# Kernel optimization log

Measured on AMD Instinct MI355X. Metric: run time of the kernel, lower is better.

The kernel has to match this reference:

```python
import jax, jax.numpy as jnp
import numpy as np

EPS = 1e-6      # eps used in token2map / map2token weight normalization
LN_EPS = 1e-5   # torch nn.LayerNorm default


def layernorm(x, w, b):
    m = jnp.mean(x, axis=-1, keepdims=True)
    xc = x - m
    v = jnp.mean(xc * xc, axis=-1, keepdims=True)
    return xc * jax.lax.rsqrt(v + LN_EPS) * w + b


def grid_index(H_init, W_init, H, W):
    # nearest-neighbor map: flattened feature-map index for each init-grid cell
    r = (jnp.arange(H_init) * H) // H_init
    c = (jnp.arange(W_init) * W) // W_init
    return (r[:, None] * W + c[None, :]).reshape(-1)  # [N_init]


def token2map(x, idx_token, H, W, H_init, W_init):
    # tokens [B,N,C] -> feature map [B,H,W,C] via weighted scatter-mean
    B, N, C = x.shape
    idx_hw = grid_index(H_init, W_init, H, W)                    # [N_init]
    counts = jnp.zeros((H * W,), x.dtype).at[idx_hw].add(1.0)    # identical across batch
    w = (1.0 / (counts + EPS))[idx_hw]                           # [N_init]
    src = jnp.take_along_axis(x, idx_token[..., None], axis=1)   # [B,N_init,C]
    out = jnp.zeros((B, H * W, C), x.dtype).at[:, idx_hw, :].add(src * w[None, :, None])
    return out.reshape(B, H, W, C)


def map2token(fmap, idx_token, N, H_init, W_init):
    # feature map [B,H,W,C] -> tokens [B,N,C]: mean of member grid cells per token
    B, H, W, C = fmap.shape
    idx_hw = grid_index(H_init, W_init, H, W)
    bidx = jnp.arange(B)[:, None]
    counts = jnp.zeros((B, N), fmap.dtype).at[bidx, idx_token].add(1.0)
    wt = jnp.take_along_axis(1.0 / (counts + EPS), idx_token, axis=1)  # [B,N_init]
    src = fmap.reshape(B, H * W, C)[:, idx_hw, :]                      # [B,N_init,C]
    return jnp.zeros((B, N, C), fmap.dtype).at[bidx, idx_token].add(src * wt[..., None])


def _forward(x, token_score, idx_token,
             norm1_w, norm1_b, q_w, q_b, kv_w, kv_b, sr_w, sr_b, srn_w, srn_b,
             proj_w, proj_b, norm2_w, norm2_b, fc1_w, fc1_b, skip_w, dw_w, dw_b,
             fc2_w, fc2_b, H, W, H_init, W_init, token_num, num_heads):
    B, N, C = x.shape
    d = C // num_heads
    scale = d ** -0.5
    sr = 2  # sr_ratio

    xn = layernorm(x, norm1_w, norm1_b)  # q_dict['x'] = norm1(x); kv_dict is q_dict

    # ---- TCFormerDynamicAttention ----
    q = (xn @ q_w + q_b).reshape(B, N, num_heads, d).transpose(0, 2, 1, 3)  # [B,h,N,d]
    tmp = jnp.concatenate([xn, token_score], axis=-1)            # [B,N,C+1]
    tmp_map = token2map(tmp, idx_token, H, W, H_init, W_init)    # [B,H,W,C+1]
    kv_map, conf_map = tmp_map[..., :C], tmp_map[..., C]
    kv = jax.lax.conv_general_dilated(kv_map, sr_w, (sr, sr), 'VALID',
        dimension_numbers=('NHWC', 'HWIO', 'NHWC')) + sr_b       # sr conv, stride 2
    M = (H // sr) * (W // sr)
    kv = layernorm(kv.reshape(B, M, C), srn_w, srn_b)
    conf = conf_map.reshape(B, H // sr, sr, W // sr, sr).mean(axis=(2, 4)).reshape(B, M)

    kv = (kv @ kv_w + kv_b).reshape(B, M, 2, num_heads, d)
    k = kv[:, :, 0].transpose(0, 2, 1, 3)                        # [B,h,M,d]
    v = kv[:, :, 1].transpose(0, 2, 1, 3)
    attn = jnp.einsum('bhnd,bhmd->bhnm', q * scale, k) + conf[:, None, None, :]
    attn = jax.nn.softmax(attn, axis=-1)
    a = jnp.einsum('bhnm,bhmd->bhnd', attn, v).transpose(0, 2, 1, 3).reshape(B, N, C)
    x = x + (a @ proj_w + proj_b)

    # ---- TCMLP ----
    h = layernorm(x, norm2_w, norm2_b) @ fc1_w + fc1_b           # [B,N,H1]
    hmap = token2map(h, idx_token, H, W, H_init, W_init)         # [B,H,W,H1]
    hmap = jax.lax.conv_general_dilated(hmap, dw_w, (1, 1), ((1, 1), (1, 1)),
        dimension_numbers=('NHWC', 'HWIO', 'NHWC'),
        feature_group_count=h.shape[-1]) + dw_b                  # depthwise 3x3
    hc = h * skip_w + map2token(hmap, idx_token, N, H_init, W_init)  # skip = dw 1x1 conv1d
    hc = jax.nn.gelu(hc, approximate=False)
    return x + (hc @ fc2_w + fc2_b)


def setup_inputs() -> dict:
    B, N, C, H1 = 8, 1568, 256, 1024
    H = W = 56
    H_init = W_init = 112
    key = jax.random.key(0)
    ks = jax.random.split(key, 16)
    r = lambda i, shape, s=0.02: jax.random.normal(ks[i], shape, jnp.float32) * s
    return {
        'x': jax.random.normal(ks[0], (B, N, C), jnp.float32),
        'token_score': jax.random.normal(ks[1], (B, N, 1), jnp.float32),
        'idx_token': jax.random.randint(ks[2], (B, H_init * W_init), 0, N),
        'norm1_w': jnp.ones((C,), jnp.float32), 'norm1_b': jnp.zeros((C,), jnp.float32),
        'q_w': r(3, (C, C)), 'q_b': jnp.zeros((C,), jnp.float32),
        'kv_w': r(4, (C, 2 * C)), 'kv_b': jnp.zeros((2 * C,), jnp.float32),
        'sr_w': r(5, (2, 2, C, C)), 'sr_b': jnp.zeros((C,), jnp.float32),
        'srn_w': jnp.ones((C,), jnp.float32), 'srn_b': jnp.zeros((C,), jnp.float32),
        'proj_w': r(6, (C, C)), 'proj_b': jnp.zeros((C,), jnp.float32),
        'norm2_w': jnp.ones((C,), jnp.float32), 'norm2_b': jnp.zeros((C,), jnp.float32),
        'fc1_w': r(7, (C, H1)), 'fc1_b': jnp.zeros((H1,), jnp.float32),
        'skip_w': 1.0 + r(8, (H1,), 0.1),
        'dw_w': r(9, (3, 3, 1, H1), 0.1), 'dw_b': jnp.zeros((H1,), jnp.float32),
        'fc2_w': r(10, (H1, C)), 'fc2_b': jnp.zeros((C,), jnp.float32),
        'H': H, 'W': W, 'H_init': H_init, 'W_init': W_init,
        'token_num': N, 'num_heads': 8,
    }


def reference(x, token_score, idx_token, norm1_w, norm1_b, q_w, q_b, kv_w, kv_b,
              sr_w, sr_b, srn_w, srn_b, proj_w, proj_b, norm2_w, norm2_b,
              fc1_w, fc1_b, skip_w, dw_w, dw_b, fc2_w, fc2_b,
              H, W, H_init, W_init, token_num, num_heads):
    return _forward(x, token_score, idx_token, norm1_w, norm1_b, q_w, q_b, kv_w, kv_b,
                    sr_w, sr_b, srn_w, srn_b, proj_w, proj_b, norm2_w, norm2_b,
                    fc1_w, fc1_b, skip_w, dw_w, dw_b, fc2_w, fc2_b,
                    H, W, H_init, W_init, token_num, num_heads)
```

## Files before the change

kernel.cpp:

```cpp
#include <hip/hip_runtime.h>
#include <math.h>

#define BB 8
#define NTOK 1568
#define CD 256
#define HIMG 56
#define WIMG 56
#define HWSZ 3136
#define HIG 112
#define WIG 112
#define NI 12544
#define MKV 784
#define MPAD 800
#define NHEADS 8
#define HEADD 32
#define HH1 1024
#define ROWS1 (BB*NTOK)
#define ROWSK (BB*MKV)
#define LOG2E 1.4426950408889634f

typedef unsigned short bfu;
typedef __attribute__((ext_vector_type(4))) unsigned short bf4;
typedef __attribute__((ext_vector_type(8))) unsigned short bf8;
typedef __attribute__((ext_vector_type(8))) short s8v;
typedef __attribute__((ext_vector_type(4))) float f4v;
typedef __attribute__((ext_vector_type(16))) float f16v;

__device__ inline float b2f(bfu u) { union { unsigned i; float f; } x; x.i = (unsigned)u << 16; return x.f; }
__device__ inline bfu f2b(float f) {
  union { float f; unsigned i; } x; x.f = f;
  unsigned r = x.i + 0x7fffu + ((x.i >> 16) & 1u);
  return (bfu)(r >> 16);
}
__device__ inline int get_isb(const unsigned* probe) { return probe[0] == 0x3F803F80u ? 1 : 0; }
__device__ inline float ldd(const void* p, size_t i, int isb) {
  return isb ? b2f(((const bfu*)p)[i]) : ((const float*)p)[i];
}
__device__ inline int xswz(int wg, int nwg) {
  return (nwg & 7) ? wg : (wg & 7) * (nwg >> 3) + (wg >> 3);
}

__global__ __launch_bounds__(256) void wtr_tile(const void* __restrict__ w0,
                                                const void* __restrict__ w1,
                                                const void* __restrict__ w2,
                                                const void* __restrict__ w3,
                                                const void* __restrict__ w4,
                                                const void* __restrict__ w5,
                                                const void* __restrict__ w6,
                                                const void* __restrict__ w7,
                                                bfu* __restrict__ wtb,
                                                bfu* __restrict__ vt,
                                                float* __restrict__ conf,
                                                const unsigned* __restrict__ probe) {
  int isb = get_isb(probe);
  int bid = blockIdx.x, tid = threadIdx.x;
  if (bid >= 1064) {
    int t = (bid - 1064) * 256 + tid;
    int b = t / 4096, rem = t % 4096;
    int d = rem / 16, m = MKV + (rem % 16);
    vt[((size_t)(b * 256 + d)) * MPAD + m] = 0;
    if (t < 128) conf[(t / 16) * MPAD + MKV + (t % 16)] = -1e30f;
    return;
  }
  if (bid >= 1024) {
    int idx = (bid - 1024) * 256 + tid;
    if (idx < 9216) wtb[1048576 + idx] = f2b(ldd(w6, idx, isb));
    else            wtb[1048576 + idx] = f2b(ldd(w7, idx - 9216, isb));
    return;
  }
  const void* W; int K, N; bfu* Wt; int tloc;
  if (bid < 64)       { W = w0; K = 256;  N = 256;  Wt = wtb;          tloc = bid; }
  else if (bid < 320) { W = w1; K = 1024; N = 256;  Wt = wtb + 65536;  tloc = bid - 64; }
  else if (bid < 448) { W = w2; K = 256;  N = 512;  Wt = wtb + 327680; tloc = bid - 320; }
  else if (bid < 512) { W = w3; K = 256;  N = 256;  Wt = wtb + 458752; tloc = bid - 448; }
  else if (bid < 768) { W = w4; K = 256;  N = 1024; Wt = wtb + 524288; tloc = bid - 512; }
  else                { W = w5; K = 1024; N = 256;  Wt = wtb + 786432; tloc = bid - 768; }
  int ntn = N >> 5;
  int tn = tloc % ntn, tk = tloc / ntn;
  int n0 = tn * 32, k0 = tk * 32;
  __shared__ float s[32][33];
  int tx = tid & 31, ty = tid >> 5;
#pragma unroll
  for (int i = 0; i < 4; i++) {
    int k = ty + 8 * i;
    s[k][tx] = ldd(W, (size_t)(k0 + k) * N + n0 + tx, isb);
  }
  __syncthreads();
#pragma unroll
  for (int i = 0; i < 4; i++) {
    int n = ty + 8 * i;
    Wt[(size_t)(n0 + n) * K + k0 + tx] = f2b(s[tx][n]);
  }
}

__global__ __launch_bounds__(256) void ln_kernel(const void* __restrict__ in, int inmode,
                                                 const void* __restrict__ w,
                                                 const void* __restrict__ bta,
                                                 bfu* __restrict__ out,
                                                 const unsigned* __restrict__ probe) {
  int isb = get_isb(probe);
  int im = (inmode == 2) ? isb : inmode;
  int blk = xswz(blockIdx.x, gridDim.x);
  int wv = threadIdx.x >> 6, lane = threadIdx.x & 63;
  int row = blk * 4 + wv;
  int c4 = lane * 4;
  float v[4];
  if (im) {
    bf4 t = *(const bf4*)((const bfu*)in + (size_t)row * CD + c4);
#pragma unroll
    for (int j = 0; j < 4; j++) v[j] = b2f(t[j]);
  } else {
    float4 t = *(const float4*)((const float*)in + (size_t)row * CD + c4);
    v[0] = t.x; v[1] = t.y; v[2] = t.z; v[3] = t.w;
  }
  float s1 = v[0] + v[1] + v[2] + v[3];
  float s2 = v[0] * v[0] + v[1] * v[1] + v[2] * v[2] + v[3] * v[3];
#pragma unroll
  for (int off = 1; off < 64; off <<= 1) {
    s1 += __shfl_xor(s1, off);
    s2 += __shfl_xor(s2, off);
  }
  float m = s1 * (1.0f / CD);
  float inv = rsqrtf(s2 * (1.0f / CD) - m * m + 1e-5f);
  bf4 ov;
#pragma unroll
  for (int j = 0; j < 4; j++)
    ov[j] = f2b((v[j] - m) * inv * ldd(w, c4 + j, isb) + ldd(bta, c4 + j, isb));
  *(bf4*)(out + (size_t)row * CD + c4) = ov;
}

__global__ __launch_bounds__(256) void gemm2ph(const bfu* __restrict__ A,
                                               const bfu* __restrict__ Bt,
                                               const void* __restrict__ bias,
                                               const void* __restrict__ resid, int rmode,
                                               void* __restrict__ Cc, int cmode,
                                               void* __restrict__ aux,
                                               int K, int Ncols,
                                               const unsigned* __restrict__ probe) {
  int isb = get_isb(probe);
  int rm = (rmode == 1) ? (isb ? 3 : 2) : rmode;
  int cm = (cmode == 2) ? (isb ? 0 : 1) : cmode;
  __shared__ bfu As[2][64][40];
  __shared__ bfu Bs[2][64][40];
  int t = threadIdx.x;
  int nbx = Ncols >> 6;
  int id = xswz(blockIdx.x, gridDim.x);
  int row0 = (id / nbx) * 64, col0 = (id % nbx) * 64;
  int sr = t >> 2, sc = (t & 3) * 8;
  int w = t >> 6, lane = t & 63;
  int li = lane & 15, q = lane >> 4;
  int wm = w * 16;
  const bfu* pa = A + (size_t)(row0 + sr) * K + sc;
  const bfu* pb = Bt + (size_t)(col0 + sr) * K + sc;
  f4v zz = {0.f, 0.f, 0.f, 0.f};
  f4v acc[4];
#pragma unroll
  for (int ni = 0; ni < 4; ni++) acc[ni] = zz;
  s8v la = *(const s8v*)(pa);
  s8v lb = *(const s8v*)(pb);
  int cur = 0;
  for (int k0 = 32; k0 <= K; k0 += 32) {
    *(s8v*)(&As[cur][sr][sc]) = la;
    *(s8v*)(&Bs[cur][sr][sc]) = lb;
    __syncthreads();
    if (k0 < K) {
      la = *(const s8v*)(pa + k0);
      lb = *(const s8v*)(pb + k0);
    }
    s8v af  = *(const s8v*)(&As[cur][wm + li][q * 8]);
    s8v bf0 = *(const s8v*)(&Bs[cur][li][q * 8]);
    s8v bf1 = *(const s8v*)(&Bs[cur][16 + li][q * 8]);
    s8v bf2 = *(const s8v*)(&Bs[cur][32 + li][q * 8]);
    s8v bf3 = *(const s8v*)(&Bs[cur][48 + li][q * 8]);
    __builtin_amdgcn_s_setprio(1);
    acc[0] = __builtin_amdgcn_mfma_f32_16x16x32_bf16(af, bf0, acc[0], 0, 0, 0);
    acc[1] = __builtin_amdgcn_mfma_f32_16x16x32_bf16(af, bf1, acc[1], 0, 0, 0);
    acc[2] = __builtin_amdgcn_mfma_f32_16x16x32_bf16(af, bf2, acc[2], 0, 0, 0);
    acc[3] = __builtin_amdgcn_mfma_f32_16x16x32_bf16(af, bf3, acc[3], 0, 0, 0);
    __builtin_amdgcn_s_setprio(0);
    cur ^= 1;
  }
  float bw[4];
#pragma unroll
  for (int ni = 0; ni < 4; ni++) bw[ni] = ldd(bias, col0 + ni * 16 + li, isb);
#pragma unroll
  for (int ni = 0; ni < 4; ni++) {
    int col = col0 + ni * 16 + li;
#pragma unroll
    for (int r = 0; r < 4; r++) {
      int row = row0 + wm + q * 4 + r;
      size_t base = (size_t)row * Ncols + col;
      float v = acc[ni][r] + bw[ni];
      if (rm == 2) v += ((const float*)resid)[base];
      else if (rm == 3) v += b2f(((const bfu*)resid)[base]);
      if (cm == 0) ((bfu*)Cc)[base] = f2b(v);
      else if (cm == 1) ((float*)Cc)[base] = v;
      else {
        if (col < 256) ((bfu*)Cc)[base] = f2b(v);
        else {
          int bb = row / MKV, mm = row - bb * MKV;
          ((bfu*)aux)[((size_t)(bb * 256) + (col - 256)) * MPAD + mm] = f2b(v);
        }
      }
    }
  }
}

__global__ __launch_bounds__(256) void akv_kernel(const bfu* __restrict__ xn,
                                                  const void* __restrict__ tscore,
                                                  const int* __restrict__ idx_token,
                                                  bfu* __restrict__ Akv,
                                                  float* __restrict__ conf,
                                                  const unsigned* __restrict__ probe) {
  int isb = get_isb(probe);
  int blk = xswz(blockIdx.x, gridDim.x), tid = threadIdx.x;
  int b = blk / MKV, m = blk % MKV;
  int i2 = m / 28, j2 = m % 28;
  __shared__ int nn[16];
  __shared__ float cacc[16];
  if (tid < 16) {
    int a = (tid >> 3) & 1, kb = (tid >> 2) & 1, di = (tid >> 1) & 1, dj = tid & 1;
    int ti = 4 * i2 + 2 * a + di, tj = 4 * j2 + 2 * kb + dj;
    int n = idx_token[b * NI + ti * WIG + tj];
    nn[tid] = n;
    cacc[tid] = ldd(tscore, b * NTOK + n, isb);
  }
  __syncthreads();
  const float w4 = 1.0f / (4.0f + 1e-6f);
  int g = tid >> 6, c4 = (tid & 63) * 4;
  bf4 a0 = *(const bf4*)(xn + (size_t)(b * NTOK + nn[g * 4 + 0]) * CD + c4);
  bf4 a1 = *(const bf4*)(xn + (size_t)(b * NTOK + nn[g * 4 + 1]) * CD + c4);
  bf4 a2 = *(const bf4*)(xn + (size_t)(b * NTOK + nn[g * 4 + 2]) * CD + c4);
  bf4 a3 = *(const bf4*)(xn + (size_t)(b * NTOK + nn[g * 4 + 3]) * CD + c4);
  bf4 rv;
#pragma unroll
  for (int j = 0; j < 4; j++)
    rv[j] = f2b(w4 * (b2f(a0[j]) + b2f(a1[j]) + b2f(a2[j]) + b2f(a3[j])));
  *(bf4*)(Akv + (size_t)blk * 1024 + g * CD + c4) = rv;
  if (tid == 0) {
    float s = 0.f;
    for (int k = 0; k < 16; k++) s += cacc[k];
    conf[b * MPAD + m] = 0.25f * w4 * s * 5.656854249492381f;
  }
}

__global__ __launch_bounds__(256) void attn_kernel(const bfu* __restrict__ qb,
                                                   const bfu* __restrict__ kv,
                                                   const bfu* __restrict__ vt,
                                                   const float* __restrict__ conf,
                                                   bfu* __restrict__ out) {
  __shared__ float sdata[4][64][17];
  int tid = threadIdx.x;
  int w = tid >> 6, lane = tid & 63;
  int l31 = lane & 31, hi = lane >> 5;
  int blk = xswz(blockIdx.x, gridDim.x);
  int qt = blk % 25, tt = blk / 25;
  int hh = tt & 7, b = tt >> 3;
  int n0 = qt * 64;
  int two = (qt < 24);
  const bfu* qrow1 = qb + (size_t)(b * NTOK + n0 + l31) * CD + hh * HEADD + hi * 8;
  s8v qfA1 = *(const s8v*)(qrow1);
  s8v qfB1 = *(const s8v*)(qrow1 + 16);
  s8v qfA2 = {0, 0, 0, 0, 0, 0, 0, 0}, qfB2 = qfA2;
  if (two) {
    const bfu* qrow2 = qrow1 + (size_t)32 * CD;
    qfA2 = *(const s8v*)(qrow2);
    qfB2 = *(const s8v*)(qrow2 + 16);
  }
  const float scale = 0.17677669529663689f * LOG2E;
  const bfu* kbase = kv + hh * HEADD + hi * 8;
  const bfu* vbase = vt + ((size_t)(b * 256 + hh * HEADD + l31)) * MPAD + hi * 8;
  const float* cbase = conf + b * MPAD + 4 * hi;
  f16v oc1, oc2;
#pragma unroll
  for (int r = 0; r < 16; r++) { oc1[r] = 0.f; oc2[r] = 0.f; }
  float lr1 = 0.f, lr2 = 0.f;
  int w32 = w * 32;
  const bfu* kp0 = kbase + (size_t)(b * MKV + w32 + l31) * 512;
  s8v kfA = *(const s8v*)(kp0);
  s8v kfB = *(const s8v*)(kp0 + 16);
  s8v vfA = *(const s8v*)(vbase + w32);
  s8v vfB = *(const s8v*)(vbase + w32 + 16);
  float4 cf0 = *(const float4*)(cbase + w32);
  float4 cf1 = *(const float4*)(cbase + w32 + 8);
  float4 cf2 = *(const float4*)(cbase + w32 + 16);
  float4 cf3 = *(const float4*)(cbase + w32 + 24);
  for (int m0 = w32; m0 < MPAD; m0 += 128) {
    s8v ckA = kfA, ckB = kfB, cvA = vfA, cvB = vfB;
    float4 d0 = cf0, d1 = cf1, d2 = cf2, d3 = cf3;
    int m1 = m0 + 128;
    if (m1 < MPAD) {
      int mA = m1 + l31; if (mA > MKV - 1) mA = MKV - 1;
      const bfu* kp = kbase + (size_t)(b * MKV + mA) * 512;
      kfA = *(const s8v*)(kp);
      kfB = *(const s8v*)(kp + 16);
      vfA = *(const s8v*)(vbase + m1);
      vfB = *(const s8v*)(vbase + m1 + 16);
      cf0 = *(const float4*)(cbase + m1);
      cf1 = *(const float4*)(cbase + m1 + 8);
      cf2 = *(const float4*)(cbase + m1 + 16);
      cf3 = *(const float4*)(cbase + m1 + 24);
    }
    f16v cseed;
    cseed[0] = d0.x; cseed[1] = d0.y; cseed[2] = d0.z; cseed[3] = d0.w;
    cseed[4] = d1.x; cseed[5] = d1.y; cseed[6] = d1.z; cseed[7] = d1.w;
    cseed[8] = d2.x; cseed[9] = d2.y; cseed[10] = d2.z; cseed[11] = d2.w;
    cseed[12] = d3.x; cseed[13] = d3.y; cseed[14] = d3.z; cseed[15] = d3.w;
    __builtin_amdgcn_s_setprio(1);
    f16v c = __builtin_amdgcn_mfma_f32_32x32x16_bf16(ckA, qfA1, cseed, 0, 0, 0);
    c = __builtin_amdgcn_mfma_f32_32x32x16_bf16(ckB, qfB1, c, 0, 0, 0);
    __builtin_amdgcn_s_setprio(0);
    {
      float p[16], ps0 = 0.f, ps1 = 0.f, ps2 = 0.f, ps3 = 0.f;
#pragma unroll
      for (int r = 0; r < 16; r++) {
        p[r] = __builtin_amdgcn_exp2f(c[r] * scale);
        if ((r & 3) == 0) ps0 += p[r];
        else if ((r & 3) == 1) ps1 += p[r];
        else if ((r & 3) == 2) ps2 += p[r];
        else ps3 += p[r];
      }
      lr1 += (ps0 + ps1) + (ps2 + ps3);
      unsigned Z[8];
#pragma unroll
      for (int a2 = 0; a2 < 8; a2++)
        asm("v_cvt_pk_bf16_f32 %0, %1, %2" : "=v"(Z[a2]) : "v"(p[2 * a2]), "v"(p[2 * a2 + 1]));
      asm("v_permlane32_swap_b32 %0, %1" : "+v"(Z[0]), "+v"(Z[2]));
      asm("v_permlane32_swap_b32 %0, %1" : "+v"(Z[1]), "+v"(Z[3]));
      asm("v_permlane32_swap_b32 %0, %1" : "+v"(Z[4]), "+v"(Z[6]));
      asm("v_permlane32_swap_b32 %0, %1" : "+v"(Z[5]), "+v"(Z[7]));
      union { unsigned u[4]; s8v v; } B1, B2;
      B1.u[0] = Z[0]; B1.u[1] = Z[1]; B1.u[2] = Z[2]; B1.u[3] = Z[3];
      B2.u[0] = Z[4]; B2.u[1] = Z[5]; B2.u[2] = Z[6]; B2.u[3] = Z[7];
      __builtin_amdgcn_s_setprio(1);
      oc1 = __builtin_amdgcn_mfma_f32_32x32x16_bf16(cvA, B1.v, oc1, 0, 0, 0);
      oc1 = __builtin_amdgcn_mfma_f32_32x32x16_bf16(cvB, B2.v, oc1, 0, 0, 0);
      __builtin_amdgcn_s_setprio(0);
    }
    if (two) {
      __builtin_amdgcn_s_setprio(1);
      f16v c2 = __builtin_amdgcn_mfma_f32_32x32x16_bf16(ckA, qfA2, cseed, 0, 0, 0);
      c2 = __builtin_amdgcn_mfma_f32_32x32x16_bf16(ckB, qfB2, c2, 0, 0, 0);
      __builtin_amdgcn_s_setprio(0);
      float p[16], ps0 = 0.f, ps1 = 0.f, ps2 = 0.f, ps3 = 0.f;
#pragma unroll
      for (int r = 0; r < 16; r++) {
        p[r] = __builtin_amdgcn_exp2f(c2[r] * scale);
        if ((r & 3) == 0) ps0 += p[r];
        else if ((r & 3) == 1) ps1 += p[r];
        else if ((r & 3) == 2) ps2 += p[r];
        else ps3 += p[r];
      }
      lr2 += (ps0 + ps1) + (ps2 + ps3);
      unsigned Z[8];
#pragma unroll
      for (int a2 = 0; a2 < 8; a2++)
        asm("v_cvt_pk_bf16_f32 %0, %1, %2" : "=v"(Z[a2]) : "v"(p[2 * a2]), "v"(p[2 * a2 + 1]));
      asm("v_permlane32_swap_b32 %0, %1" : "+v"(Z[0]), "+v"(Z[2]));
      asm("v_permlane32_swap_b32 %0, %1" : "+v"(Z[1]), "+v"(Z[3]));
      asm("v_permlane32_swap_b32 %0, %1" : "+v"(Z[4]), "+v"(Z[6]));
      asm("v_permlane32_swap_b32 %0, %1" : "+v"(Z[5]), "+v"(Z[7]));
      union { unsigned u[4]; s8v v; } B1, B2;
      B1.u[0] = Z[0]; B1.u[1] = Z[1]; B1.u[2] = Z[2]; B1.u[3] = Z[3];
      B2.u[0] = Z[4]; B2.u[1] = Z[5]; B2.u[2] = Z[6]; B2.u[3] = Z[7];
      __builtin_amdgcn_s_setprio(1);
      oc2 = __builtin_amdgcn_mfma_f32_32x32x16_bf16(cvA, B1.v, oc2, 0, 0, 0);
      oc2 = __builtin_amdgcn_mfma_f32_32x32x16_bf16(cvB, B2.v, oc2, 0, 0, 0);
      __builtin_amdgcn_s_setprio(0);
    }
  }
#pragma unroll
  for (int r = 0; r < 16; r++) sdata[w][lane][r] = oc1[r];
  sdata[w][lane][16] = lr1;
  __syncthreads();
  if (w == 0) {
    float s[17];
#pragma unroll
    for (int r = 0; r < 17; r++)
      s[r] = sdata[0][lane][r] + sdata[1][lane][r] + sdata[2][lane][r] + sdata[3][lane][r];
    float l = s[16];
    l += __shfl_xor(l, 32);
    float inv = 1.0f / l;
    bfu* op = out + (size_t)(b * NTOK + n0 + l31) * CD + hh * HEADD + 4 * hi;
#pragma unroll
    for (int g = 0; g < 4; g++) {
      bf4 o;
#pragma unroll
      for (int u = 0; u < 4; u++) o[u] = f2b(s[4 * g + u] * inv);
      *(bf4*)(op + 8 * g) = o;
    }
  }
  if (two) {
    __syncthreads();
#pragma unroll
    for (int r = 0; r < 16; r++) sdata[w][lane][r] = oc2[r];
    sdata[w][lane][16] = lr2;
    __syncthreads();
    if (w == 0) {
      float s[17];
#pragma unroll
      for (int r = 0; r < 17; r++)
        s[r] = sdata[0][lane][r] + sdata[1][lane][r] + sdata[2][lane][r] + sdata[3][lane][r];
      float l = s[16];
      l += __shfl_xor(l, 32);
      float inv = 1.0f / l;
      bfu* op = out + (size_t)(b * NTOK + n0 + 32 + l31) * CD + hh * HEADD + 4 * hi;
#pragma unroll
      for (int g = 0; g < 4; g++) {
        bf4 o;
#pragma unroll
        for (int u = 0; u < 4; u++) o[u] = f2b(s[4 * g + u] * inv);
        *(bf4*)(op + 8 * g) = o;
      }
    }
  }
}

__global__ __launch_bounds__(128) void hmap_kernel(const bfu* __restrict__ h,
                                                   const int* __restrict__ idx_token,
                                                   bfu* __restrict__ hmap) {
  int blk = xswz(blockIdx.x, gridDim.x), tid = threadIdx.x;
  int b = blk / HWSZ, cell = blk % HWSZ;
  int i = cell / WIMG, j = cell % WIMG;
  __shared__ int nn[4];
  if (tid < 4) {
    int di = tid >> 1, dj = tid & 1;
    nn[tid] = idx_token[b * NI + (2 * i + di) * WIG + (2 * j + dj)];
  }
  __syncthreads();
  const float w4 = 1.0f / (4.0f + 1e-6f);
  int c8 = tid * 8;
  bf8 a0 = *(const bf8*)(h + (size_t)(b * NTOK + nn[0]) * HH1 + c8);
  bf8 a1 = *(const bf8*)(h + (size_t)(b * NTOK + nn[1]) * HH1 + c8);
  bf8 a2 = *(const bf8*)(h + (size_t)(b * NTOK + nn[2]) * HH1 + c8);
  bf8 a3 = *(const bf8*)(h + (size_t)(b * NTOK + nn[3]) * HH1 + c8);
  bf8 rv;
#pragma unroll
  for (int j2 = 0; j2 < 8; j2++)
    rv[j2] = f2b(w4 * (b2f(a0[j2]) + b2f(a1[j2]) + b2f(a2[j2]) + b2f(a3[j2])));
  *(bf8*)(hmap + (size_t)blk * HH1 + c8) = rv;
}

__global__ __launch_bounds__(256) void dw_kernel(const bfu* __restrict__ hmap,
                                                 const bfu* __restrict__ dwt,
                                                 const bfu* __restrict__ dbt,
                                                 bfu* __restrict__ dwout) {
  int blk = xswz(blockIdx.x, gridDim.x);
  int j4 = blk % 14; int rem = blk / 14;
  int i = rem % HIMG; int b = rem / HIMG;
  int tid = threadIdx.x;
  int c4 = tid * 4;
  int j0 = j4 * 4;
  float wf[9][4];
#pragma unroll
  for (int k = 0; k < 9; k++) {
    bf4 wv = *(const bf4*)(dwt + k * HH1 + c4);
#pragma unroll
    for (int u = 0; u < 4; u++) wf[k][u] = b2f(wv[u]);
  }
  bf4 bias = *(const bf4*)(dbt + c4);
  float bi[4];
#pragma unroll
  for (int u = 0; u < 4; u++) bi[u] = b2f(bias[u]);
  bf4 tp[3][6];
  const size_t bbase = (size_t)b * HWSZ;
#pragma unroll
  for (int r = 0; r < 3; r++) {
    int yy = i - 1 + r;
    bool rowok = (unsigned)yy < (unsigned)HIMG;
#pragma unroll
    for (int cc = 0; cc < 6; cc++) {
      int xx = j0 - 1 + cc;
      bf4 v = {0, 0, 0, 0};
      if (rowok && (unsigned)xx < (unsigned)WIMG)
        v = *(const bf4*)(hmap + (bbase + yy * WIMG + xx) * HH1 + c4);
      tp[r][cc] = v;
    }
  }
#pragma unroll
  for (int j = 0; j < 4; j++) {
    float acc[4] = {bi[0], bi[1], bi[2], bi[3]};
#pragma unroll
    for (int r = 0; r < 3; r++)
#pragma unroll
      for (int kx = 0; kx < 3; kx++) {
        bf4 hv = tp[r][j + kx];
#pragma unroll
        for (int u = 0; u < 4; u++) acc[u] += b2f(hv[u]) * wf[r * 3 + kx][u];
      }
    bf4 ov;
#pragma unroll
    for (int u = 0; u < 4; u++) ov[u] = f2b(acc[u]);
    *(bf4*)(dwout + (bbase + i * WIMG + j0 + j) * HH1 + c4) = ov;
  }
}

__global__ void count_kernel(const int* __restrict__ idx, int* __restrict__ cnt) {
  int t = xswz(blockIdx.x, gridDim.x) * 256 + threadIdx.x;
  int b = t / NI;
  atomicAdd(&cnt[b * NTOK + idx[t]], 1);
}
__global__ __launch_bounds__(256) void scan_kernel(const int* __restrict__ cnt, int2* __restrict__ co) {
  int b = blockIdx.x, tid = threadIdx.x;
  __shared__ int s[NTOK];
  for (int i = tid; i < NTOK; i += 256) s[i] = cnt[b * NTOK + i];
  __syncthreads();
  for (int st = 1; st < NTOK; st <<= 1) {
    int vals[7]; int k = 0;
    for (int i = tid; i < NTOK; i += 256, k++) vals[k] = (i >= st) ? s[i - st] : 0;
    __syncthreads();
    k = 0;
    for (int i = tid; i < NTOK; i += 256, k++) s[i] += vals[k];
    __syncthreads();
  }
  for (int i = tid; i < NTOK; i += 256) {
    int2 v; v.x = cnt[b * NTOK + i]; v.y = (i > 0) ? s[i - 1] : 0;
    co[b * NTOK + i] = v;
  }
}
__global__ void fill_kernel(const int* __restrict__ idx, const int2* __restrict__ co,
                            int* __restrict__ cursor, int* __restrict__ tlist) {
  int t = xswz(blockIdx.x, gridDim.x) * 256 + threadIdx.x;
  int b = t / NI, tt = t % NI;
  int n = idx[t];
  int p = atomicAdd(&cursor[b * NTOK + n], 1);
  tlist[b * NI + co[b * NTOK + n].y + p] = tt;
}

__global__ __launch_bounds__(128) void m2t_kernel(const bfu* __restrict__ h,
                                                  const bfu* __restrict__ dwout,
                                                  const int2* __restrict__ co,
                                                  const int* __restrict__ tlist,
                                                  const void* __restrict__ skipw,
                                                  bfu* __restrict__ hc,
                                                  const unsigned* __restrict__ probe) {
  int isb = get_isb(probe);
  int blk = xswz(blockIdx.x, gridDim.x), tid = threadIdx.x;
  int lane = tid & 63;
  int b = blk / NTOK, n = blk % NTOK;
  int c8 = tid * 8;
  bf8 hv = *(const bf8*)(h + (size_t)blk * HH1 + c8);
  int2 cv = co[b * NTOK + n];
  int c = cv.x, o0 = cv.y;
  float inv = 1.0f / ((float)c + 1e-6f);
  float a[8] = {};
  for (int k0 = 0; k0 < c; k0 += 16) {
    int kk = k0 + (lane & 15);
    int e = 0;
    if (kk < c) e = tlist[b * NI + o0 + kk];
    bf8 dv[16];
#pragma unroll
    for (int j = 0; j < 16; j++) {
      if (k0 + j < c) {
        int tt = __shfl(e, j);
        int ti = tt / WIG, tj = tt % WIG;
        int cell = (ti >> 1) * WIMG + (tj >> 1);
        dv[j] = *(const bf8*)(dwout + ((size_t)b * HWSZ + cell) * HH1 + c8);
      }
    }
#pragma unroll
    for (int j = 0; j < 16; j++) {
      if (k0 + j < c) {
#pragma unroll
        for (int j2 = 0; j2 < 8; j2++) a[j2] += b2f(dv[j][j2]);
      }
    }
  }
  bf8 ov;
  const float is2 = 0.70710678118654752f;
#pragma unroll
  for (int j2 = 0; j2 < 8; j2++) {
    float r = b2f(hv[j2]) * ldd(skipw, c8 + j2, isb) + a[j2] * inv;
    r = 0.5f * r * (1.0f + erff(r * is2));
    ov[j2] = f2b(r);
  }
  *(bf8*)(hc + (size_t)blk * HH1 + c8) = ov;
}

extern "C" void kernel_launch(void* const* d_in, const int* in_sizes, int n_in,
                              void* d_out, int out_size, void* d_ws, size_t ws_size,
                              hipStream_t stream) {
  const void* x        = d_in[0];
  const void* tscore   = d_in[1];
  const int*  idx_tok  = (const int*)d_in[2];
  const void* norm1_w  = d_in[3];
  const void* norm1_b  = d_in[4];
  const void* q_w      = d_in[5];
  const void* q_b      = d_in[6];
  const void* kv_w     = d_in[7];
  const void* kv_b     = d_in[8];
  const void* sr_w     = d_in[9];
  const void* sr_b     = d_in[10];
  const void* srn_w    = d_in[11];
  const void* srn_b    = d_in[12];
  const void* proj_w   = d_in[13];
  const void* proj_b   = d_in[14];
  const void* norm2_w  = d_in[15];
  const void* norm2_b  = d_in[16];
  const void* fc1_w    = d_in[17];
  const void* fc1_b    = d_in[18];
  const void* skip_w   = d_in[19];
  const void* dw_w     = d_in[20];
  const void* dw_b     = d_in[21];
  const void* fc2_w    = d_in[22];
  const void* fc2_b    = d_in[23];
  const unsigned* probe = (const unsigned*)d_in[3];

  float* ws = (float*)d_ws;
  size_t o = 0;
  float* x2 = ws + o;          o += (size_t)ROWS1 * CD;
  float* hR = ws + o;          o += (size_t)ROWS1 * HH1 / 2;
  float* mR = ws + o;          o += (size_t)BB * HWSZ * HH1 / 2;
  float* dR = ws + o;          o += (size_t)BB * HWSZ * HH1 / 2;
  int* ibase = (int*)(ws + o); o += (size_t)(4 * ROWS1 + BB * NI);
  bfu* wtb   = (bfu*)(ws + o); o += 529408;
  bfu* vtb   = (bfu*)(ws + o);

  bfu* Akv   = (bfu*)hR;
  bfu* kvc   = (bfu*)(hR + (size_t)ROWSK * 1024 / 2);
  bfu* h     = (bfu*)hR;
  bfu* qbuf  = (bfu*)mR;
  bfu* kvout = (bfu*)(mR + (size_t)ROWS1 * CD / 2);
  float* conf  = mR + (size_t)ROWS1 * CD / 2 + (size_t)ROWSK * 512 / 2;
  bfu* hmap  = (bfu*)mR;
  bfu* hc    = (bfu*)mR;
  bfu* xn    = (bfu*)dR;
  bfu* dwout = (bfu*)dR;
  int* counts = ibase;
  int* cursor = ibase + ROWS1;
  int2* co2   = (int2*)(ibase + 2 * ROWS1);
  int* tlist  = ibase + 4 * ROWS1;
  bfu* q_wt    = wtb;
  bfu* sr_wt   = wtb + 65536;
  bfu* kv_wt   = wtb + 327680;
  bfu* proj_wt = wtb + 458752;
  bfu* fc1_wt  = wtb + 524288;
  bfu* fc2_wt  = wtb + 786432;
  bfu* dwt     = wtb + 1048576;
  bfu* dbt     = wtb + 1057792;

  wtr_tile<<<1192, 256, 0, stream>>>(q_w, sr_w, kv_w, proj_w, fc1_w, fc2_w, dw_w, dw_b,
                                     wtb, vtb, conf, probe);
  hipMemsetAsync(counts, 0, (size_t)(2 * ROWS1) * sizeof(int), stream);

  ln_kernel<<<ROWS1 / 4, 256, 0, stream>>>(x, 2, norm1_w, norm1_b, xn, probe);
  gemm2ph<<<784, 256, 0, stream>>>(xn, q_wt, q_b, nullptr, 0, qbuf, 0, nullptr, 256, 256, probe);
  akv_kernel<<<ROWSK, 256, 0, stream>>>(xn, tscore, idx_tok, Akv, conf, probe);
  gemm2ph<<<392, 256, 0, stream>>>(Akv, sr_wt, sr_b, nullptr, 0, kvc, 0, nullptr, 1024, 256, probe);
  ln_kernel<<<ROWSK / 4, 256, 0, stream>>>(kvc, 1, srn_w, srn_b, kvc, probe);
  gemm2ph<<<784, 256, 0, stream>>>(kvc, kv_wt, kv_b, nullptr, 0, kvout, 3, vtb, 256, 512, probe);
  attn_kernel<<<BB * NHEADS * 25, 256, 0, stream>>>(qbuf, kvout, vtb, conf, xn);
  gemm2ph<<<784, 256, 0, stream>>>(xn, proj_wt, proj_b, x, 1, x2, 1, nullptr, 256, 256, probe);
  ln_kernel<<<ROWS1 / 4, 256, 0, stream>>>(x2, 0, norm2_w, norm2_b, xn, probe);
  gemm2ph<<<3136, 256, 0, stream>>>(xn, fc1_wt, fc1_b, nullptr, 0, h, 0, nullptr, 256, 1024, probe);
  hmap_kernel<<<BB * HWSZ, 128, 0, stream>>>(h, idx_tok, hmap);
  dw_kernel<<<BB * HIMG * 14, 256, 0, stream>>>(hmap, dwt, dbt, dwout);
  count_kernel<<<(BB * NI) / 256, 256, 0, stream>>>(idx_tok, counts);
  scan_kernel<<<BB, 256, 0, stream>>>(counts, co2);
  fill_kernel<<<(BB * NI) / 256, 256, 0, stream>>>(idx_tok, co2, cursor, tlist);
  m2t_kernel<<<ROWS1, 128, 0, stream>>>(h, dwout, co2, tlist, skip_w, hc, probe);
  gemm2ph<<<784, 256, 0, stream>>>(hc, fc2_wt, fc2_b, x2, 2, d_out, 2, nullptr, 1024, 256, probe);
}
```

Measured before the change: 412.9 us.

## Merge independent kernels into combined launches and simplify m2t gather loop

Fuses independent stages into single launches by block-index dispatch: the q-projection GEMM with the kv-pooling kernel, the hmap gather with the token-count atomics, and the depthwise conv with the per-batch scan. The aim is to remove several kernel launches and the idle gaps between them, letting independent work fill the GPU together. The m2t gather loop also moves from 16 buffered loads per batch to 8 loads accumulated directly, which lowers register pressure but leaves fewer loads in flight. Mixing heterogeneous blocks in one kernel forces the shared-memory and register footprint to the maximum of both bodies, which can reduce occupancy.

```diff
diff --git a/kernel.cpp b/kernel.cpp
--- a/kernel.cpp
+++ b/kernel.cpp
@@ -129,22 +129,18 @@
   *(bf4*)(out + (size_t)row * CD + c4) = ov;
 }
 
-__global__ __launch_bounds__(256) void gemm2ph(const bfu* __restrict__ A,
-                                               const bfu* __restrict__ Bt,
-                                               const void* __restrict__ bias,
-                                               const void* __restrict__ resid, int rmode,
-                                               void* __restrict__ Cc, int cmode,
-                                               void* __restrict__ aux,
-                                               int K, int Ncols,
-                                               const unsigned* __restrict__ probe) {
-  int isb = get_isb(probe);
-  int rm = (rmode == 1) ? (isb ? 3 : 2) : rmode;
-  int cm = (cmode == 2) ? (isb ? 0 : 1) : cmode;
+__device__ inline void gemm2ph_body(int id,
+                                    const bfu* __restrict__ A,
+                                    const bfu* __restrict__ Bt,
+                                    const void* __restrict__ bias,
+                                    const void* __restrict__ resid, int rm,
+                                    void* __restrict__ Cc, int cm,
+                                    void* __restrict__ aux,
+                                    int K, int Ncols, int isb) {
   __shared__ bfu As[2][64][40];
   __shared__ bfu Bs[2][64][40];
   int t = threadIdx.x;
   int nbx = Ncols >> 6;
-  int id = xswz(blockIdx.x, gridDim.x);
   int row0 = (id / nbx) * 64, col0 = (id % nbx) * 64;
   int sr = t >> 2, sc = (t & 3) * 8;
   int w = t >> 6, lane = t & 63;
@@ -206,14 +202,27 @@
   }
 }
 
-__global__ __launch_bounds__(256) void akv_kernel(const bfu* __restrict__ xn,
-                                                  const void* __restrict__ tscore,
-                                                  const int* __restrict__ idx_token,
-                                                  bfu* __restrict__ Akv,
-                                                  float* __restrict__ conf,
-                                                  const unsigned* __restrict__ probe) {
+__global__ __launch_bounds__(256) void gemm2ph(const bfu* __restrict__ A,
+                                               const bfu* __restrict__ Bt,
+                                               const void* __restrict__ bias,
+                                               const void* __restrict__ resid, int rmode,
+                                               void* __restrict__ Cc, int cmode,
+                                               void* __restrict__ aux,
+                                               int K, int Ncols,
+                                               const unsigned* __restrict__ probe) {
   int isb = get_isb(probe);
-  int blk = xswz(blockIdx.x, gridDim.x), tid = threadIdx.x;
+  int rm = (rmode == 1) ? (isb ? 3 : 2) : rmode;
+  int cm = (cmode == 2) ? (isb ? 0 : 1) : cmode;
+  gemm2ph_body(xswz(blockIdx.x, gridDim.x), A, Bt, bias, resid, rm, Cc, cm, aux, K, Ncols, isb);
+}
+
+__device__ inline void akv_body(int blk,
+                                const bfu* __restrict__ xn,
+                                const void* __restrict__ tscore,
+                                const int* __restrict__ idx_token,
+                                bfu* __restrict__ Akv,
+                                float* __restrict__ conf, int isb) {
+  int tid = threadIdx.x;
   int b = blk / MKV, m = blk % MKV;
   int i2 = m / 28, j2 = m % 28;
   __shared__ int nn[16];
@@ -242,6 +251,22 @@
     for (int k = 0; k < 16; k++) s += cacc[k];
     conf[b * MPAD + m] = 0.25f * w4 * s * 5.656854249492381f;
   }
+}
+
+__global__ __launch_bounds__(256) void qakv_kernel(const bfu* __restrict__ xn,
+                                                   const bfu* __restrict__ q_wt,
+                                                   const void* __restrict__ q_b,
+                                                   bfu* __restrict__ qbuf,
+                                                   const void* __restrict__ tscore,
+                                                   const int* __restrict__ idx_token,
+                                                   bfu* __restrict__ Akv,
+                                                   float* __restrict__ conf,
+                                                   const unsigned* __restrict__ probe) {
+  int isb = get_isb(probe);
+  if (blockIdx.x < 784)
+    gemm2ph_body(xswz(blockIdx.x, 784), xn, q_wt, q_b, nullptr, 0, qbuf, 0, nullptr, 256, 256, isb);
+  else
+    akv_body(xswz(blockIdx.x - 784, 6272), xn, tscore, idx_token, Akv, conf, isb);
 }
 
 __global__ __launch_bounds__(256) void attn_kernel(const bfu* __restrict__ qb,
@@ -416,10 +441,10 @@
   }
 }
 
-__global__ __launch_bounds__(128) void hmap_kernel(const bfu* __restrict__ h,
-                                                   const int* __restrict__ idx_token,
-                                                   bfu* __restrict__ hmap) {
-  int blk = xswz(blockIdx.x, gridDim.x), tid = threadIdx.x;
+__device__ inline void hmap_body(int blk, const bfu* __restrict__ h,
+                                 const int* __restrict__ idx_token,
+                                 bfu* __restrict__ hmap) {
+  int tid = threadIdx.x;
   int b = blk / HWSZ, cell = blk % HWSZ;
   int i = cell / WIMG, j = cell % WIMG;
   __shared__ int nn[4];
@@ -441,11 +466,23 @@
   *(bf8*)(hmap + (size_t)blk * HH1 + c8) = rv;
 }
 
-__global__ __launch_bounds__(256) void dw_kernel(const bfu* __restrict__ hmap,
-                                                 const bfu* __restrict__ dwt,
-                                                 const bfu* __restrict__ dbt,
-                                                 bfu* __restrict__ dwout) {
-  int blk = xswz(blockIdx.x, gridDim.x);
+__global__ __launch_bounds__(128) void hmapcnt_kernel(const bfu* __restrict__ h,
+                                                      const int* __restrict__ idx_token,
+                                                      bfu* __restrict__ hmap,
+                                                      int* __restrict__ cnt) {
+  if (blockIdx.x < 25088) {
+    hmap_body(xswz(blockIdx.x, 25088), h, idx_token, hmap);
+  } else {
+    int t = xswz(blockIdx.x - 25088, 784) * 128 + threadIdx.x;
+    int b = t / NI;
+    atomicAdd(&cnt[b * NTOK + idx_token[t]], 1);
+  }
+}
+
+__device__ inline void dw_body(int blk, const bfu* __restrict__ hmap,
+                               const bfu* __restrict__ dwt,
+                               const bfu* __restrict__ dbt,
+                               bfu* __restrict__ dwout) {
   int j4 = blk % 14; int rem = blk / 14;
   int i = rem % HIMG; int b = rem / HIMG;
   int tid = threadIdx.x;
@@ -495,13 +532,8 @@
   }
 }
 
-__global__ void count_kernel(const int* __restrict__ idx, int* __restrict__ cnt) {
-  int t = xswz(blockIdx.x, gridDim.x) * 256 + threadIdx.x;
-  int b = t / NI;
-  atomicAdd(&cnt[b * NTOK + idx[t]], 1);
-}
-__global__ __launch_bounds__(256) void scan_kernel(const int* __restrict__ cnt, int2* __restrict__ co) {
-  int b = blockIdx.x, tid = threadIdx.x;
+__device__ inline void scan_body(int b, const int* __restrict__ cnt, int2* __restrict__ co) {
+  int tid = threadIdx.x;
   __shared__ int s[NTOK];
   for (int i = tid; i < NTOK; i += 256) s[i] = cnt[b * NTOK + i];
   __syncthreads();
@@ -518,6 +550,17 @@
     co[b * NTOK + i] = v;
   }
 }
+
+__global__ __launch_bounds__(256) void dwscan_kernel(const bfu* __restrict__ hmap,
+                                                     const bfu* __restrict__ dwt,
+                                                     const bfu* __restrict__ dbt,
+                                                     bfu* __restrict__ dwout,
+                                                     const int* __restrict__ cnt,
+                                                     int2* __restrict__ co) {
+  if (blockIdx.x < 6272) dw_body(xswz(blockIdx.x, 6272), hmap, dwt, dbt, dwout);
+  else scan_body(blockIdx.x - 6272, cnt, co);
+}
+
 __global__ void fill_kernel(const int* __restrict__ idx, const int2* __restrict__ co,
                             int* __restrict__ cursor, int* __restrict__ tlist) {
   int t = xswz(blockIdx.x, gridDim.x) * 256 + threadIdx.x;
@@ -544,25 +587,19 @@
   int c = cv.x, o0 = cv.y;
   float inv = 1.0f / ((float)c + 1e-6f);
   float a[8] = {};
-  for (int k0 = 0; k0 < c; k0 += 16) {
-    int kk = k0 + (lane & 15);
+  for (int k0 = 0; k0 < c; k0 += 8) {
+    int kk = k0 + (lane & 7);
     int e = 0;
     if (kk < c) e = tlist[b * NI + o0 + kk];
-    bf8 dv[16];
-#pragma unroll
-    for (int j = 0; j < 16; j++) {
+#pragma unroll
+    for (int j = 0; j < 8; j++) {
       if (k0 + j < c) {
         int tt = __shfl(e, j);
         int ti = tt / WIG, tj = tt % WIG;
         int cell = (ti >> 1) * WIMG + (tj >> 1);
-        dv[j] = *(const bf8*)(dwout + ((size_t)b * HWSZ + cell) * HH1 + c8);
-      }
-    }
-#pragma unroll
-    for (int j = 0; j < 16; j++) {
-      if (k0 + j < c) {
-#pragma unroll
-        for (int j2 = 0; j2 < 8; j2++) a[j2] += b2f(dv[j][j2]);
+        bf8 dv = *(const bf8*)(dwout + ((size_t)b * HWSZ + cell) * HH1 + c8);
+#pragma unroll
+        for (int j2 = 0; j2 < 8; j2++) a[j2] += b2f(dv[j2]);
       }
     }
   }
@@ -644,8 +681,7 @@
   hipMemsetAsync(counts, 0, (size_t)(2 * ROWS1) * sizeof(int), stream);
 
   ln_kernel<<<ROWS1 / 4, 256, 0, stream>>>(x, 2, norm1_w, norm1_b, xn, probe);
-  gemm2ph<<<784, 256, 0, stream>>>(xn, q_wt, q_b, nullptr, 0, qbuf, 0, nullptr, 256, 256, probe);
-  akv_kernel<<<ROWSK, 256, 0, stream>>>(xn, tscore, idx_tok, Akv, conf, probe);
+  qakv_kernel<<<7056, 256, 0, stream>>>(xn, q_wt, q_b, qbuf, tscore, idx_tok, Akv, conf, probe);
   gemm2ph<<<392, 256, 0, stream>>>(Akv, sr_wt, sr_b, nullptr, 0, kvc, 0, nullptr, 1024, 256, probe);
   ln_kernel<<<ROWSK / 4, 256, 0, stream>>>(kvc, 1, srn_w, srn_b, kvc, probe);
   gemm2ph<<<784, 256, 0, stream>>>(kvc, kv_wt, kv_b, nullptr, 0, kvout, 3, vtb, 256, 512, probe);
@@ -653,10 +689,8 @@
   gemm2ph<<<784, 256, 0, stream>>>(xn, proj_wt, proj_b, x, 1, x2, 1, nullptr, 256, 256, probe);
   ln_kernel<<<ROWS1 / 4, 256, 0, stream>>>(x2, 0, norm2_w, norm2_b, xn, probe);
   gemm2ph<<<3136, 256, 0, stream>>>(xn, fc1_wt, fc1_b, nullptr, 0, h, 0, nullptr, 256, 1024, probe);
-  hmap_kernel<<<BB * HWSZ, 128, 0, stream>>>(h, idx_tok, hmap);
-  dw_kernel<<<BB * HIMG * 14, 256, 0, stream>>>(hmap, dwt, dbt, dwout);
-  count_kernel<<<(BB * NI) / 256, 256, 0, stream>>>(idx_tok, counts);
-  scan_kernel<<<BB, 256, 0, stream>>>(counts, co2);
+  hmapcnt_kernel<<<25872, 128, 0, stream>>>(h, idx_tok, hmap, counts);
+  dwscan_kernel<<<6280, 256, 0, stream>>>(hmap, dwt, dbt, dwout, counts, co2);
   fill_kernel<<<(BB * NI) / 256, 256, 0, stream>>>(idx_tok, co2, cursor, tlist);
   m2t_kernel<<<ROWS1, 128, 0, stream>>>(h, dwout, co2, tlist, skip_w, hc, probe);
   gemm2ph<<<784, 256, 0, stream>>>(hc, fc2_wt, fc2_b, x2, 2, d_out, 2, nullptr, 1024, 256, probe);
```

Result: faster. 404.2 us (-2.1%).
